# Optimization experiments

Measured on AMD Instinct MI355X. Metric: run time of the kernel, lower is better.

The kernel has to match this reference:

```python
import jax, jax.numpy as jnp
import numpy as np
jax.config.update("jax_enable_x64", True)  # faithful int64 spatial hashing as in torch

T = 524288            # hash table size per level
NL = jnp.asarray([16, 22, 30, 42, 58, 80, 110, 152, 209, 288, 397, 547, 754, 1039, 1432, 1974], dtype=jnp.float32)
L = 16
SCALE = 3.0
L_EMBED = 4
PI2 = 2654435761
PI3 = 805459861
NPTS = 524288

_k = np.arange(8)
# ceil/floor selector per original vertex enumeration, axis order (x, y, z)
CEIL_BITS = jnp.asarray(np.stack([
    [0, 1, 0, 0, 0, 1, 1, 1],   # x uses ceil
    [0, 0, 1, 0, 1, 0, 1, 1],   # y uses ceil
    [0, 0, 0, 1, 1, 1, 0, 1],   # z uses ceil
], axis=-1).astype(bool))        # [8,3]
# grid_sample places vertex k at grid (d,h,w)=(k//4,(k//2)%2,k%2); with align_corners=False
# on a 2x2x2 grid and grid coord frac-0.5, the weight for index 1 along W/H/D is frac_x/frac_y/frac_z.
# (This faithfully reproduces the original's vertex/weight mismatch.)
WEIGHT_BITS = jnp.asarray(np.stack([_k % 2, (_k // 2) % 2, _k // 4], axis=-1).astype(bool))  # [8,3]


def hash_features(xu, tables):
    # xu: [N,3] in ~[0,1]; tables: [L,T,2]
    def level(_, xs):
        n, table = xs
        p = xu * n
        pf = jnp.floor(p)
        pc = jnp.ceil(p)
        frac = p - pf                                                        # [N,3]
        verts = jnp.where(CEIL_BITS[None], pc[:, None, :], pf[:, None, :]).astype(jnp.int64)  # [N,8,3]
        h = ((verts[..., 0] * 1) ^ (verts[..., 1] * PI2) ^ (verts[..., 2] * PI3)) % T          # [N,8]
        w = jnp.prod(jnp.where(WEIGHT_BITS[None], frac[:, None, :], 1.0 - frac[:, None, :]), axis=-1)  # [N,8]
        feat = jnp.einsum('nk,nkf->nf', w.astype(table.dtype), table[h])    # [N,2]
        return None, feat
    _, feats = jax.lax.scan(level, None, (NL, tables))                       # [L,N,2]
    return jnp.transpose(feats, (1, 0, 2)).reshape(xu.shape[0], -1)          # [N,2L]


def posenc(d):
    outs = [d]
    for i in range(L_EMBED):
        s = (2.0 ** i) * d
        outs.append(jnp.sin(s))
        outs.append(jnp.cos(s))
    return jnp.concatenate(outs, -1)  # [N, 3+6*L_EMBED]


def setup_inputs() -> dict:
    key = jax.random.key(0)
    ks = jax.random.split(key, 16)
    f32 = jnp.float32
    s = 0.05
    return {
        "x": jax.random.normal(ks[0], (NPTS, 3), f32),
        "d": jax.random.normal(ks[1], (NPTS, 3), f32),
        "tables": (jax.random.uniform(ks[2], (L, T, 2), f32) * 2.0 - 1.0) * 1e-4,
        "w1a": jax.random.normal(ks[3], (2 * L, 64), f32) * s,
        "b1a": jnp.zeros((64,), f32),
        "w1b": jax.random.normal(ks[4], (64, 16), f32) * s,
        "b1b": jnp.zeros((16,), f32),
        "w2a": jax.random.normal(ks[5], (16 + 3 + 6 * L_EMBED, 64), f32) * s,
        "b2a": jnp.zeros((64,), f32),
        "w2b": jax.random.normal(ks[6], (64, 64), f32) * s,
        "b2b": jnp.zeros((64,), f32),
        "w2c": jax.random.normal(ks[7], (64, 3), f32) * s,
        "b2c": jnp.zeros((3,), f32),
    }


def reference(x, d, tables, w1a, b1a, w1b, b1b, w2a, b2a, w2b, b2b, w2c, b2c):
    xs = x / SCALE
    mask = (jnp.abs(xs[:, 0]) < 0.5) & (jnp.abs(xs[:, 1]) < 0.5) & (jnp.abs(xs[:, 2]) < 0.5)
    xu = xs + 0.5
    feats = hash_features(xu, tables)                     # [N, 32]
    h = jax.nn.relu(feats @ w1a + b1a) @ w1b + b1b        # [N, 16]
    log_sigma = jnp.where(mask, h[:, 0], -100000.0)
    z = jnp.concatenate([h, posenc(d)], -1)               # [N, 43]
    z = jax.nn.relu(z @ w2a + b2a)
    z = jax.nn.relu(z @ w2b + b2b)
    c = jax.nn.sigmoid(z @ w2c + b2c)
    color = jnp.where(mask[:, None], c, 0.0)
    return color, jnp.exp(log_sigma)
```

## Files before the change

kernel.cpp:

```cpp
#include <hip/hip_runtime.h>
#include <math.h>

#define NPTS 524288
#define HALF (NPTS / 2)
#define TSZ  524288
#define TMASK (TSZ - 1)
#define FP8SCALE 4096.0f
#define FP8INV   (1.0f / 4096.0f)

typedef __attribute__((ext_vector_type(8))) short v8s;
typedef __attribute__((ext_vector_type(4))) float v4f;
typedef __attribute__((ext_vector_type(2))) float v2f;

#define MFMA16(a, b, c) __builtin_amdgcn_mfma_f32_16x16x32_bf16(a, b, c, 0, 0, 0)

__device__ __constant__ float NLf[16] = {
    16.f, 22.f, 30.f, 42.f, 58.f, 80.f, 110.f, 152.f,
    209.f, 288.f, 397.f, 547.f, 754.f, 1039.f, 1432.f, 1974.f
};

#define CEILX 0xE2
#define CEILY 0xD4
#define CEILZ 0xB8

__device__ __forceinline__ short bf16r(float v) {
    unsigned b = __float_as_uint(v);
    b += 0x7FFFu + ((b >> 16) & 1u);
    return (short)(b >> 16);
}
__device__ __forceinline__ unsigned packbf(float a, float b) {
    return (unsigned)(unsigned short)bf16r(a) | ((unsigned)(unsigned short)bf16r(b) << 16);
}
__device__ __forceinline__ unsigned sel4(uint4 t, unsigned i) {
    const unsigned ab = (i & 1u) ? t.y : t.x;
    const unsigned cd = (i & 1u) ? t.w : t.z;
    return (i & 2u) ? cd : ab;
}
__device__ __forceinline__ unsigned sel8(uint4 t, unsigned i) {
    const unsigned w = sel4(t, i >> 1);
    return (i & 1u) ? (w >> 16) : (w & 0xFFFFu);
}

__global__ __launch_bounds__(256) void pack_tables(
    const float4* __restrict__ tbl, unsigned* __restrict__ out,
    unsigned* __restrict__ idxbuf, unsigned* __restrict__ cnt)
{
    const int idx = blockIdx.x * 256 + threadIdx.x;
    const float4 t = tbl[idx];
    const unsigned lo = (unsigned)__builtin_amdgcn_cvt_pk_fp8_f32(
                            t.x * FP8SCALE, t.y * FP8SCALE, 0, false) & 0xFFFFu;
    const unsigned hi = (unsigned)__builtin_amdgcn_cvt_pk_fp8_f32(
                            t.z * FP8SCALE, t.w * FP8SCALE, 0, false) & 0xFFFFu;
    out[idx] = lo | (hi << 16);
    if (idx < NPTS) idxbuf[idx] = 0xFFFFFFFFu;
    if (idx == 0) cnt[0] = 0u;
}

__global__ __launch_bounds__(1024) void ngp_compact2(
    const float* __restrict__ x, const float* __restrict__ d,
    unsigned* __restrict__ idxbuf, float* __restrict__ xc,
    float* __restrict__ dc, unsigned* __restrict__ cnt,
    float* __restrict__ out)
{
    __shared__ unsigned sWCnt[16];
    __shared__ unsigned sBase;

    const int tid  = threadIdx.x;
    const int wv   = tid >> 6, lane = tid & 63;
    const int i    = blockIdx.x * 1024 + tid;

    const float x0 = x[3*i+0], x1 = x[3*i+1], x2 = x[3*i+2];
    const float xs0 = x0 / 3.0f, xs1 = x1 / 3.0f, xs2 = x2 / 3.0f;
    const bool act = (fabsf(xs0) < 0.5f) && (fabsf(xs1) < 0.5f) && (fabsf(xs2) < 0.5f);
    if (!act) {
        out[3*i+0] = 0.f; out[3*i+1] = 0.f; out[3*i+2] = 0.f;
        out[3*NPTS + i] = 0.f;
    }
    const unsigned long long mb = __ballot(act);
    if (lane == 0) sWCnt[wv] = (unsigned)__popcll(mb);
    __syncthreads();
    if (tid == 0) {
        unsigned tot = 0;
        #pragma unroll
        for (int w = 0; w < 16; ++w) tot += sWCnt[w];
        sBase = atomicAdd(cnt, tot);
    }
    __syncthreads();
    if (act) {
        unsigned off = sBase;
        for (int w = 0; w < wv; ++w) off += sWCnt[w];
        off += (unsigned)__popcll(mb & ((1ull << lane) - 1ull));
        idxbuf[off] = (unsigned)i;
        xc[3*off+0] = x0; xc[3*off+1] = x1; xc[3*off+2] = x2;
        dc[3*off+0] = d[3*i+0]; dc[3*off+1] = d[3*i+1]; dc[3*off+2] = d[3*i+2];
    }
}

__global__ __launch_bounds__(256) void ngp_hash6(
    const float* __restrict__ xc, const unsigned short* __restrict__ tables_pk,
    const unsigned* __restrict__ cnt, unsigned* __restrict__ feats_pk)
{
    __shared__ float sX[768];
    const int NC = (int)cnt[0];
    if (blockIdx.x * 256 >= NC) return;

    const int tid = threadIdx.x;
    const int l = blockIdx.y;
    const float n = NLf[l];
    const unsigned short* tbl = tables_pk + (size_t)l * TSZ;

    for (int r = tid; r < 768; r += 256)
        sX[r] = xc[(size_t)blockIdx.x * 768 + r];
    __syncthreads();

    const int j = blockIdx.x * 256 + tid;
    const float xu0 = sX[tid * 3 + 0] / 3.0f + 0.5f;
    const float xu1 = sX[tid * 3 + 1] / 3.0f + 0.5f;
    const float xu2 = sX[tid * 3 + 2] / 3.0f + 0.5f;

    const float p0 = xu0 * n, p1 = xu1 * n, p2 = xu2 * n;
    const float f0 = floorf(p0), f1 = floorf(p1), f2 = floorf(p2);
    const float fr0 = p0 - f0, fr1 = p1 - f1, fr2 = p2 - f2;
    const float g0 = 1.f - fr0, g1 = 1.f - fr1, g2 = 1.f - fr2;
    const unsigned uvf0 = (unsigned)(int)f0;
    const unsigned uvc0 = (unsigned)(int)ceilf(p0);
    const unsigned syf = (unsigned)(int)f1 * 2654435761u;
    const unsigned syc = (unsigned)(int)ceilf(p1) * 2654435761u;
    const unsigned szf = (unsigned)(int)f2 * 805459861u;
    const unsigned szc = (unsigned)(int)ceilf(p2) * 805459861u;

    const float w0 = g0 * g1 * g2,  w1 = fr0 * g1 * g2;
    const float w2 = g0 * fr1 * g2, w6 = g0 * fr1 * fr2;
    const float w3 = fr0 * fr1 * g2, w5 = fr0 * g1 * fr2;
    const float w4 = g0 * g1 * fr2, w7 = fr0 * fr1 * fr2;

    const unsigned Ss[4] = { syf ^ szf, syc ^ szf, syf ^ szc, syc ^ szc };
    const float wf[4] = { w0, w2, w3, w4 };
    const float wc[4] = { w1, w6, w5, w7 };

    float a0 = 0.f, a1 = 0.f;
    #pragma unroll
    for (int pr = 0; pr < 4; ++pr) {
        const unsigned hf = (Ss[pr] ^ uvf0) & TMASK;
        const unsigned hc = (Ss[pr] ^ uvc0) & TMASK;
        const unsigned diff = hf ^ hc;
        const uint4 tv = *(const uint4*)(tbl + (hf & ~7u));
        const unsigned ef = sel8(tv, hf & 7u);
        unsigned ec;
        if (diff <= 7u) ec = sel8(tv, hc & 7u);
        else            ec = (unsigned)tbl[hc];
        const v2f ff = __builtin_amdgcn_cvt_pk_f32_fp8((int)ef, false);
        const v2f fc = __builtin_amdgcn_cvt_pk_f32_fp8((int)ec, false);
        a0 = fmaf(wf[pr], ff.x, a0);
        a1 = fmaf(wf[pr], ff.y, a1);
        a0 = fmaf(wc[pr], fc.x, a0);
        a1 = fmaf(wc[pr], fc.y, a1);
    }
    a0 *= FP8INV;
    a1 *= FP8INV;
    feats_pk[(size_t)l * NPTS + j] = packbf(a0, a1);
}

#define PZ 72
#define SWL(row) ((((row) >> 2) & 3) << 4)

__global__ __launch_bounds__(512) void ngp_mlp5(
    const float* __restrict__ dc,
    const unsigned* __restrict__ feats_pk, const unsigned* __restrict__ idxbuf,
    const unsigned* __restrict__ cnt,
    const float* __restrict__ w1a, const float* __restrict__ b1a,
    const float* __restrict__ w1b, const float* __restrict__ b1b,
    const float* __restrict__ w2a, const float* __restrict__ b2a,
    const float* __restrict__ w2b, const float* __restrict__ b2b,
    const float* __restrict__ w2c, const float* __restrict__ b2c,
    float* __restrict__ out)
{
    __shared__ short sW1a[64 * 40];
    __shared__ short sW1b[16 * 72];
    __shared__ short sW2a[64 * 72];
    __shared__ short sW2b[64 * 72];
    __shared__ short sW2c[16 * 72];
    __shared__ short sZ[8 * 16 * PZ];

    const int NC = (int)cnt[0];
    if (blockIdx.x * 128 >= NC) return;

    const int tid = threadIdx.x;

    for (int idx = tid; idx < 32 * 64; idx += 512) {
        const int k = idx >> 6, n2 = idx & 63;
        sW1a[n2 * 40 + k] = bf16r(w1a[k * 64 + n2]);
    }
    for (int idx = tid; idx < 64 * 16; idx += 512) {
        const int k = idx >> 4, n2 = idx & 15;
        sW1b[n2 * 72 + k] = bf16r(w1b[k * 16 + n2]);
    }
    for (int idx = tid; idx < 64 * 64; idx += 512) {
        const int k = idx >> 6, n2 = idx & 63;
        sW2a[n2 * 72 + k] = bf16r(k < 43 ? w2a[k * 64 + n2] : 0.f);
    }
    for (int idx = tid; idx < 64 * 64; idx += 512) {
        const int k = idx >> 6, n2 = idx & 63;
        sW2b[n2 * 72 + k] = bf16r(w2b[k * 64 + n2]);
    }
    for (int idx = tid; idx < 64 * 16; idx += 512) {
        const int k = idx >> 4, n2 = idx & 15;
        sW2c[n2 * 72 + k] = bf16r(n2 < 3 ? w2c[k * 3 + n2] : 0.f);
    }
    __syncthreads();

    const int wave = tid >> 6, lane = tid & 63;
    const int m = lane & 15, q = lane >> 4;
    short* zb = &sZ[wave * 16 * PZ];

    const int j0 = (blockIdx.x * 8 + wave) * 16;
    if (j0 >= NC) return;

    float bb1a[4], bb2a[4], bb2b[4];
    #pragma unroll
    for (int ct = 0; ct < 4; ++ct) {
        bb1a[ct] = b1a[ct * 16 + m];
        bb2a[ct] = b2a[ct * 16 + m];
        bb2b[ct] = b2b[ct * 16 + m];
    }
    const float bb1b = b1b[m];
    const float bb2c = (m < 3) ? b2c[m] : 0.f;

    #pragma unroll
    for (int it = 0; it < 4; ++it) {
        const int l = it * 4 + q;
        *(unsigned*)(zb + m * PZ + ((2 * l) ^ SWL(m))) =
            feats_pk[(size_t)l * NPTS + j0 + m];
    }

    {
        const v8s a0 = *(const v8s*)(zb + m * PZ + ((q * 8) ^ SWL(m)));
        #pragma unroll
        for (int ct = 0; ct < 4; ++ct) {
            const float bv = bb1a[ct];
            v4f acc = {bv, bv, bv, bv};
            acc = MFMA16(a0, *(const v8s*)(sW1a + (ct * 16 + m) * 40 + q * 8), acc);
            #pragma unroll
            for (int r = 0; r < 4; ++r)
                zb[(q * 4 + r) * PZ + ((ct * 16 + m) ^ (q << 4))] = bf16r(fmaxf(acc[r], 0.f));
        }
    }

    v4f hacc;
    {
        const v8s a10 = *(const v8s*)(zb + m * PZ + ((q * 8) ^ SWL(m)));
        const v8s a11 = *(const v8s*)(zb + m * PZ + ((32 + q * 8) ^ SWL(m)));
        v4f hv = {bb1b, bb1b, bb1b, bb1b};
        hv = MFMA16(a10, *(const v8s*)(sW1b + m * 72 + q * 8), hv);
        hv = MFMA16(a11, *(const v8s*)(sW1b + m * 72 + 32 + q * 8), hv);
        hacc = hv;
        #pragma unroll
        for (int r = 0; r < 4; ++r)
            zb[(q * 4 + r) * PZ + (m ^ (q << 4))] = bf16r(hv[r]);
    }

    {
        const float dd0 = dc[3*(j0+m)+0], dd1 = dc[3*(j0+m)+1], dd2 = dc[3*(j0+m)+2];
        v8s pk;
        #pragma unroll
        for (int jj = 0; jj < 8; ++jj) {
            const int k = 16 + q * 8 + jj;
            float v;
            if (k < 19) {
                v = (k == 16) ? dd0 : ((k == 17) ? dd1 : dd2);
            } else if (k < 43) {
                const int idx = k - 19;
                const int e = idx / 6, w = idx - 6 * e;
                const float base = (w == 0 || w == 3) ? dd0 : ((w == 1 || w == 4) ? dd1 : dd2);
                const float s = (float)(1 << e) * base;
                v = (w < 3) ? __sinf(s) : __cosf(s);
            } else {
                v = 0.f;
            }
            pk[jj] = bf16r(v);
        }
        *(v8s*)(zb + m * PZ + ((16 + q * 8) ^ SWL(m))) = pk;
        *(unsigned long long*)(zb + m * PZ + ((48 + q * 4) ^ SWL(m))) = 0ull;
    }

    {
        const v8s a20 = *(const v8s*)(zb + m * PZ + ((q * 8) ^ SWL(m)));
        const v8s a21 = *(const v8s*)(zb + m * PZ + ((32 + q * 8) ^ SWL(m)));
        #pragma unroll
        for (int ct = 0; ct < 4; ++ct) {
            const float bv = bb2a[ct];
            v4f acc = {bv, bv, bv, bv};
            acc = MFMA16(a20, *(const v8s*)(sW2a + (ct * 16 + m) * 72 + q * 8), acc);
            acc = MFMA16(a21, *(const v8s*)(sW2a + (ct * 16 + m) * 72 + 32 + q * 8), acc);
            #pragma unroll
            for (int r = 0; r < 4; ++r)
                zb[(q * 4 + r) * PZ + ((ct * 16 + m) ^ (q << 4))] = bf16r(fmaxf(acc[r], 0.f));
        }
    }

    {
        const v8s a20 = *(const v8s*)(zb + m * PZ + ((q * 8) ^ SWL(m)));
        const v8s a21 = *(const v8s*)(zb + m * PZ + ((32 + q * 8) ^ SWL(m)));
        #pragma unroll
        for (int ct = 0; ct < 4; ++ct) {
            const float bv = bb2b[ct];
            v4f acc = {bv, bv, bv, bv};
            acc = MFMA16(a20, *(const v8s*)(sW2b + (ct * 16 + m) * 72 + q * 8), acc);
            acc = MFMA16(a21, *(const v8s*)(sW2b + (ct * 16 + m) * 72 + 32 + q * 8), acc);
            #pragma unroll
            for (int r = 0; r < 4; ++r)
                zb[(q * 4 + r) * PZ + ((ct * 16 + m) ^ (q << 4))] = bf16r(fmaxf(acc[r], 0.f));
        }
    }

    {
        const v8s a30 = *(const v8s*)(zb + m * PZ + ((q * 8) ^ SWL(m)));
        const v8s a31 = *(const v8s*)(zb + m * PZ + ((32 + q * 8) ^ SWL(m)));
        v4f cacc = {bb2c, bb2c, bb2c, bb2c};
        cacc = MFMA16(a30, *(const v8s*)(sW2c + m * 72 + q * 8), cacc);
        cacc = MFMA16(a31, *(const v8s*)(sW2c + m * 72 + 32 + q * 8), cacc);

        if (m < 3) {
            #pragma unroll
            for (int r = 0; r < 4; ++r) {
                const unsigned pj = idxbuf[j0 + q * 4 + r];
                if (pj < (unsigned)NPTS) {
                    const float cv = 1.0f / (1.0f + __expf(-cacc[r]));
                    out[3 * pj + m] = cv;
                }
            }
        }
        if (m == 0) {
            #pragma unroll
            for (int r = 0; r < 4; ++r) {
                const unsigned pj = idxbuf[j0 + q * 4 + r];
                if (pj < (unsigned)NPTS)
                    out[3 * NPTS + pj] = __expf(hacc[r]);
            }
        }
    }
}

__global__ __launch_bounds__(256) void ngp_fused(
    const float* __restrict__ x, const float* __restrict__ d,
    const float* __restrict__ tables,
    const float* __restrict__ w1a, const float* __restrict__ b1a,
    const float* __restrict__ w1b, const float* __restrict__ b1b,
    const float* __restrict__ w2a, const float* __restrict__ b2a,
    const float* __restrict__ w2b, const float* __restrict__ b2b,
    const float* __restrict__ w2c, const float* __restrict__ b2c,
    float* __restrict__ out)
{
    const int i = blockIdx.x * 256 + threadIdx.x;
    if (i >= NPTS) return;
    const float xs0 = x[3*i+0] / 3.0f;
    const float xs1 = x[3*i+1] / 3.0f;
    const float xs2 = x[3*i+2] / 3.0f;
    const bool mask = (fabsf(xs0) < 0.5f) & (fabsf(xs1) < 0.5f) & (fabsf(xs2) < 0.5f);
    const float xu0 = xs0 + 0.5f, xu1 = xs1 + 0.5f, xu2 = xs2 + 0.5f;

    float feats[32];
    #pragma unroll
    for (int l = 0; l < 16; ++l) {
        const float n = NLf[l];
        const float p0 = xu0 * n, p1 = xu1 * n, p2 = xu2 * n;
        const float f0 = floorf(p0), f1 = floorf(p1), f2 = floorf(p2);
        const float fr0 = p0 - f0, fr1 = p1 - f1, fr2 = p2 - f2;
        const int vf0 = (int)f0, vf1 = (int)f1, vf2 = (int)f2;
        const int vc0 = (int)ceilf(p0), vc1 = (int)ceilf(p1), vc2 = (int)ceilf(p2);
        const float2* tbl = (const float2*)(tables + (size_t)l * (TSZ * 2));
        float a0 = 0.f, a1 = 0.f;
        #pragma unroll
        for (int k = 0; k < 8; ++k) {
            const unsigned vx = (unsigned)(((CEILX >> k) & 1) ? vc0 : vf0);
            const unsigned vy = (unsigned)(((CEILY >> k) & 1) ? vc1 : vf1);
            const unsigned vz = (unsigned)(((CEILZ >> k) & 1) ? vc2 : vf2);
            const unsigned h = (vx ^ (vy * 2654435761u) ^ (vz * 805459861u)) & TMASK;
            const float wx = (k & 1)        ? fr0 : 1.0f - fr0;
            const float wy = ((k >> 1) & 1) ? fr1 : 1.0f - fr1;
            const float wz = ((k >> 2) & 1) ? fr2 : 1.0f - fr2;
            const float wgt = wx * wy * wz;
            const float2 t = tbl[h];
            a0 = fmaf(wgt, t.x, a0);
            a1 = fmaf(wgt, t.y, a1);
        }
        feats[2*l] = a0; feats[2*l+1] = a1;
    }

    float h2v[16];
    #pragma unroll
    for (int j = 0; j < 16; ++j) h2v[j] = b1b[j];
    #pragma unroll
    for (int c = 0; c < 4; ++c) {
        float h1c[16];
        #pragma unroll
        for (int jj = 0; jj < 16; ++jj) h1c[jj] = b1a[16*c + jj];
        #pragma unroll
        for (int i2 = 0; i2 < 32; ++i2) {
            const float f = feats[i2];
            #pragma unroll
            for (int jj = 0; jj < 16; ++jj)
                h1c[jj] = fmaf(f, w1a[i2*64 + 16*c + jj], h1c[jj]);
        }
        #pragma unroll
        for (int jj = 0; jj < 16; ++jj) {
            const float f = fmaxf(h1c[jj], 0.f);
            #pragma unroll
            for (int t = 0; t < 16; ++t)
                h2v[t] = fmaf(f, w1b[(16*c + jj)*16 + t], h2v[t]);
        }
    }

    float z1[64];
    #pragma unroll
    for (int j = 0; j < 64; ++j) z1[j] = b2a[j];
    #pragma unroll
    for (int i2 = 0; i2 < 16; ++i2) {
        const float f = h2v[i2];
        #pragma unroll
        for (int j = 0; j < 64; ++j) z1[j] = fmaf(f, w2a[i2*64 + j], z1[j]);
    }
    const float d0 = d[3*i+0], d1 = d[3*i+1], d2 = d[3*i+2];
    {
        const float* r = w2a + 16*64;
        #pragma unroll
        for (int j = 0; j < 64; ++j) z1[j] = fmaf(d0, r[j], z1[j]);
        r = w2a + 17*64;
        #pragma unroll
        for (int j = 0; j < 64; ++j) z1[j] = fmaf(d1, r[j], z1[j]);
        r = w2a + 18*64;
        #pragma unroll
        for (int j = 0; j < 64; ++j) z1[j] = fmaf(d2, r[j], z1[j]);
    }
    #pragma unroll
    for (int e = 0; e < 4; ++e) {
        const float mm = (float)(1 << e);
        const float dv[3] = {d0, d1, d2};
        #pragma unroll
        for (int a = 0; a < 3; ++a) {
            const float sv = __sinf(mm * dv[a]);
            const float* rs = w2a + (19 + 6*e + a)*64;
            #pragma unroll
            for (int j = 0; j < 64; ++j) z1[j] = fmaf(sv, rs[j], z1[j]);
        }
        #pragma unroll
        for (int a = 0; a < 3; ++a) {
            const float cv = __cosf(mm * dv[a]);
            const float* rc = w2a + (19 + 6*e + 3 + a)*64;
            #pragma unroll
            for (int j = 0; j < 64; ++j) z1[j] = fmaf(cv, rc[j], z1[j]);
        }
    }
    #pragma unroll
    for (int j = 0; j < 64; ++j) z1[j] = fmaxf(z1[j], 0.f);

    float ca = b2c[0], cb = b2c[1], cc = b2c[2];
    #pragma unroll
    for (int jc = 0; jc < 64; jc += 16) {
        float acc[16];
        #pragma unroll
        for (int jj = 0; jj < 16; ++jj) acc[jj] = b2b[jc + jj];
        #pragma unroll
        for (int i2 = 0; i2 < 64; ++i2) {
            const float f = z1[i2];
            #pragma unroll
            for (int jj = 0; jj < 16; ++jj)
                acc[jj] = fmaf(f, w2b[i2*64 + jc + jj], acc[jj]);
        }
        #pragma unroll
        for (int jj = 0; jj < 16; ++jj) {
            const float v = fmaxf(acc[jj], 0.f);
            ca = fmaf(v, w2c[(jc + jj)*3 + 0], ca);
            cb = fmaf(v, w2c[(jc + jj)*3 + 1], cb);
            cc = fmaf(v, w2c[(jc + jj)*3 + 2], cc);
        }
    }

    float r = 1.0f / (1.0f + __expf(-ca));
    float g = 1.0f / (1.0f + __expf(-cb));
    float b = 1.0f / (1.0f + __expf(-cc));
    float sigma;
    if (mask) { sigma = __expf(h2v[0]); }
    else { r = 0.f; g = 0.f; b = 0.f; sigma = 0.f; }
    out[3*i + 0] = r;
    out[3*i + 1] = g;
    out[3*i + 2] = b;
    out[3*NPTS + i] = sigma;
}

extern "C" void kernel_launch(void* const* d_in, const int* in_sizes, int n_in,
                              void* d_out, int out_size, void* d_ws, size_t ws_size,
                              hipStream_t stream) {
    const float* x      = (const float*)d_in[0];
    const float* d      = (const float*)d_in[1];
    const float* tables = (const float*)d_in[2];
    const float* w1a    = (const float*)d_in[3];
    const float* b1a    = (const float*)d_in[4];
    const float* w1b    = (const float*)d_in[5];
    const float* b1b    = (const float*)d_in[6];
    const float* w2a    = (const float*)d_in[7];
    const float* b2a    = (const float*)d_in[8];
    const float* w2b    = (const float*)d_in[9];
    const float* b2b    = (const float*)d_in[10];
    const float* w2c    = (const float*)d_in[11];
    const float* b2c    = (const float*)d_in[12];
    float* out = (float*)d_out;

    const size_t need = (size_t)32 * NPTS * 4;
    if (ws_size >= need) {
        unsigned* base      = (unsigned*)d_ws;
        unsigned* feats_pk  = base;
        unsigned* tables_pk = base + (size_t)16 * NPTS;
        unsigned* idxbuf    = base + (size_t)24 * NPTS;
        unsigned* cnt       = base + (size_t)25 * NPTS;
        float*    xc        = (float*)(base + (size_t)26 * NPTS);
        float*    dc        = (float*)(base + (size_t)29 * NPTS);

        dim3 gp(16 * TSZ / (256 * 2)), bp(256);
        hipLaunchKernelGGL(pack_tables, gp, bp, 0, stream,
                           (const float4*)tables, tables_pk, idxbuf, cnt);

        dim3 gc(NPTS / 1024), bc(1024);
        hipLaunchKernelGGL(ngp_compact2, gc, bc, 0, stream,
                           x, d, idxbuf, xc, dc, cnt, out);

        dim3 gh(NPTS / 256, 16), bh(256);
        hipLaunchKernelGGL(ngp_hash6, gh, bh, 0, stream,
                           xc, (const unsigned short*)tables_pk, cnt, feats_pk);

        dim3 gm(NPTS / 128), bm(512);
        hipLaunchKernelGGL(ngp_mlp5, gm, bm, 0, stream,
                           dc, feats_pk, idxbuf, cnt, w1a, b1a, w1b, b1b,
                           w2a, b2a, w2b, b2b, w2c, b2c, out);
    } else {
        dim3 grid(NPTS / 256), block(256);
        hipLaunchKernelGGL(ngp_fused, grid, block, 0, stream,
                           x, d, tables, w1a, b1a, w1b, b1b,
                           w2a, b2a, w2b, b2b, w2c, b2c, out);
    }
}
```

Measured before the change: 268.7 us.

## Prepack MLP weights to bf16 once and loop multiple tiles per wave

Adds a small kernel that converts and transposes all MLP weights into a padded bf16 buffer, so each MLP block fills its shared memory with straight vector copies instead of strided float reads plus conversion. The MLP kernel now has each wave process four 16-point tiles in a loop, cutting the grid by four and spreading the weight-load cost over more points. This costs an extra kernel launch and fewer blocks, which may lower occupancy and latency hiding in the MLP stage.

```diff
diff --git a/kernel.cpp b/kernel.cpp
--- a/kernel.cpp
+++ b/kernel.cpp
@@ -54,6 +54,40 @@
     out[idx] = lo | (hi << 16);
     if (idx < NPTS) idxbuf[idx] = 0xFFFFFFFFu;
     if (idx == 0) cnt[0] = 0u;
+}
+
+#define W1A_OFF 0
+#define W1B_OFF 2560
+#define W2A_OFF 3712
+#define W2B_OFF 8320
+#define W2C_OFF 12928
+#define WPK_TOT 14080
+
+__global__ __launch_bounds__(1024) void ngp_packw(
+    const float* __restrict__ w1a, const float* __restrict__ w1b,
+    const float* __restrict__ w2a, const float* __restrict__ w2b,
+    const float* __restrict__ w2c, unsigned short* __restrict__ wpk)
+{
+    const int s = blockIdx.x * 1024 + threadIdx.x;
+    if (s >= WPK_TOT) return;
+    float v = 0.f;
+    if (s < W1B_OFF) {
+        const int r = s - W1A_OFF, n = r / 40, k = r % 40;
+        v = (k < 32) ? w1a[k * 64 + n] : 0.f;
+    } else if (s < W2A_OFF) {
+        const int r = s - W1B_OFF, n = r / 72, k = r % 72;
+        v = (k < 64) ? w1b[k * 16 + n] : 0.f;
+    } else if (s < W2B_OFF) {
+        const int r = s - W2A_OFF, n = r / 72, k = r % 72;
+        v = (k < 43) ? w2a[k * 64 + n] : 0.f;
+    } else if (s < W2C_OFF) {
+        const int r = s - W2B_OFF, n = r / 72, k = r % 72;
+        v = (k < 64) ? w2b[k * 64 + n] : 0.f;
+    } else {
+        const int r = s - W2C_OFF, n = r / 72, k = r % 72;
+        v = (k < 64 && n < 3) ? w2c[k * 3 + n] : 0.f;
+    }
+    wpk[s] = (unsigned short)bf16r(v);
 }
 
 __global__ __launch_bounds__(1024) void ngp_compact2(
@@ -164,57 +198,35 @@
 #define PZ 72
 #define SWL(row) ((((row) >> 2) & 3) << 4)
 
-__global__ __launch_bounds__(512) void ngp_mlp5(
+__global__ __launch_bounds__(512) void ngp_mlp6(
     const float* __restrict__ dc,
     const unsigned* __restrict__ feats_pk, const unsigned* __restrict__ idxbuf,
-    const unsigned* __restrict__ cnt,
-    const float* __restrict__ w1a, const float* __restrict__ b1a,
-    const float* __restrict__ w1b, const float* __restrict__ b1b,
-    const float* __restrict__ w2a, const float* __restrict__ b2a,
-    const float* __restrict__ w2b, const float* __restrict__ b2b,
-    const float* __restrict__ w2c, const float* __restrict__ b2c,
+    const unsigned* __restrict__ cnt, const unsigned short* __restrict__ wpk,
+    const float* __restrict__ b1a, const float* __restrict__ b1b,
+    const float* __restrict__ b2a, const float* __restrict__ b2b,
+    const float* __restrict__ b2c,
     float* __restrict__ out)
 {
-    __shared__ short sW1a[64 * 40];
-    __shared__ short sW1b[16 * 72];
-    __shared__ short sW2a[64 * 72];
-    __shared__ short sW2b[64 * 72];
-    __shared__ short sW2c[16 * 72];
+    __shared__ short sW[WPK_TOT];
     __shared__ short sZ[8 * 16 * PZ];
 
     const int NC = (int)cnt[0];
-    if (blockIdx.x * 128 >= NC) return;
+    if (blockIdx.x * 512 >= NC) return;
 
     const int tid = threadIdx.x;
-
-    for (int idx = tid; idx < 32 * 64; idx += 512) {
-        const int k = idx >> 6, n2 = idx & 63;
-        sW1a[n2 * 40 + k] = bf16r(w1a[k * 64 + n2]);
-    }
-    for (int idx = tid; idx < 64 * 16; idx += 512) {
-        const int k = idx >> 4, n2 = idx & 15;
-        sW1b[n2 * 72 + k] = bf16r(w1b[k * 16 + n2]);
-    }
-    for (int idx = tid; idx < 64 * 64; idx += 512) {
-        const int k = idx >> 6, n2 = idx & 63;
-        sW2a[n2 * 72 + k] = bf16r(k < 43 ? w2a[k * 64 + n2] : 0.f);
-    }
-    for (int idx = tid; idx < 64 * 64; idx += 512) {
-        const int k = idx >> 6, n2 = idx & 63;
-        sW2b[n2 * 72 + k] = bf16r(w2b[k * 64 + n2]);
-    }
-    for (int idx = tid; idx < 64 * 16; idx += 512) {
-        const int k = idx >> 4, n2 = idx & 15;
-        sW2c[n2 * 72 + k] = bf16r(n2 < 3 ? w2c[k * 3 + n2] : 0.f);
-    }
+    for (int i = tid; i < WPK_TOT / 8; i += 512)
+        ((uint4*)sW)[i] = ((const uint4*)wpk)[i];
     __syncthreads();
+
+    const short* sW1a = sW + W1A_OFF;
+    const short* sW1b = sW + W1B_OFF;
+    const short* sW2a = sW + W2A_OFF;
+    const short* sW2b = sW + W2B_OFF;
+    const short* sW2c = sW + W2C_OFF;
 
     const int wave = tid >> 6, lane = tid & 63;
     const int m = lane & 15, q = lane >> 4;
     short* zb = &sZ[wave * 16 * PZ];
-
-    const int j0 = (blockIdx.x * 8 + wave) * 16;
-    if (j0 >= NC) return;
 
     float bb1a[4], bb2a[4], bb2b[4];
     #pragma unroll
@@ -226,116 +238,123 @@
     const float bb1b = b1b[m];
     const float bb2c = (m < 3) ? b2c[m] : 0.f;
 
-    #pragma unroll
-    for (int it = 0; it < 4; ++it) {
-        const int l = it * 4 + q;
-        *(unsigned*)(zb + m * PZ + ((2 * l) ^ SWL(m))) =
-            feats_pk[(size_t)l * NPTS + j0 + m];
-    }
-
-    {
-        const v8s a0 = *(const v8s*)(zb + m * PZ + ((q * 8) ^ SWL(m)));
-        #pragma unroll
-        for (int ct = 0; ct < 4; ++ct) {
-            const float bv = bb1a[ct];
-            v4f acc = {bv, bv, bv, bv};
-            acc = MFMA16(a0, *(const v8s*)(sW1a + (ct * 16 + m) * 40 + q * 8), acc);
+    const int base = (blockIdx.x * 8 + wave) * 64;
+
+    for (int t = 0; t < 4; ++t) {
+        const int j0 = base + t * 16;
+        if (j0 >= NC) break;
+
+        #pragma unroll
+        for (int it = 0; it < 4; ++it) {
+            const int l = it * 4 + q;
+            *(unsigned*)(zb + m * PZ + ((2 * l) ^ SWL(m))) =
+                feats_pk[(size_t)l * NPTS + j0 + m];
+        }
+
+        {
+            const v8s a0 = *(const v8s*)(zb + m * PZ + ((q * 8) ^ SWL(m)));
+            #pragma unroll
+            for (int ct = 0; ct < 4; ++ct) {
+                const float bv = bb1a[ct];
+                v4f acc = {bv, bv, bv, bv};
+                acc = MFMA16(a0, *(const v8s*)(sW1a + (ct * 16 + m) * 40 + q * 8), acc);
+                #pragma unroll
+                for (int r = 0; r < 4; ++r)
+                    zb[(q * 4 + r) * PZ + ((ct * 16 + m) ^ (q << 4))] = bf16r(fmaxf(acc[r], 0.f));
+            }
+        }
+
+        v4f hacc;
+        {
+            const v8s a10 = *(const v8s*)(zb + m * PZ + ((q * 8) ^ SWL(m)));
+            const v8s a11 = *(const v8s*)(zb + m * PZ + ((32 + q * 8) ^ SWL(m)));
+            v4f hv = {bb1b, bb1b, bb1b, bb1b};
+            hv = MFMA16(a10, *(const v8s*)(sW1b + m * 72 + q * 8), hv);
+            hv = MFMA16(a11, *(const v8s*)(sW1b + m * 72 + 32 + q * 8), hv);
+            hacc = hv;
             #pragma unroll
             for (int r = 0; r < 4; ++r)
-                zb[(q * 4 + r) * PZ + ((ct * 16 + m) ^ (q << 4))] = bf16r(fmaxf(acc[r], 0.f));
-        }
-    }
-
-    v4f hacc;
-    {
-        const v8s a10 = *(const v8s*)(zb + m * PZ + ((q * 8) ^ SWL(m)));
-        const v8s a11 = *(const v8s*)(zb + m * PZ + ((32 + q * 8) ^ SWL(m)));
-        v4f hv = {bb1b, bb1b, bb1b, bb1b};
-        hv = MFMA16(a10, *(const v8s*)(sW1b + m * 72 + q * 8), hv);
-        hv = MFMA16(a11, *(const v8s*)(sW1b + m * 72 + 32 + q * 8), hv);
-        hacc = hv;
-        #pragma unroll
-        for (int r = 0; r < 4; ++r)
-            zb[(q * 4 + r) * PZ + (m ^ (q << 4))] = bf16r(hv[r]);
-    }
-
-    {
-        const float dd0 = dc[3*(j0+m)+0], dd1 = dc[3*(j0+m)+1], dd2 = dc[3*(j0+m)+2];
-        v8s pk;
-        #pragma unroll
-        for (int jj = 0; jj < 8; ++jj) {
-            const int k = 16 + q * 8 + jj;
-            float v;
-            if (k < 19) {
-                v = (k == 16) ? dd0 : ((k == 17) ? dd1 : dd2);
-            } else if (k < 43) {
-                const int idx = k - 19;
-                const int e = idx / 6, w = idx - 6 * e;
-                const float base = (w == 0 || w == 3) ? dd0 : ((w == 1 || w == 4) ? dd1 : dd2);
-                const float s = (float)(1 << e) * base;
-                v = (w < 3) ? __sinf(s) : __cosf(s);
-            } else {
-                v = 0.f;
+                zb[(q * 4 + r) * PZ + (m ^ (q << 4))] = bf16r(hv[r]);
+        }
+
+        {
+            const float dd0 = dc[3*(j0+m)+0], dd1 = dc[3*(j0+m)+1], dd2 = dc[3*(j0+m)+2];
+            v8s pk;
+            #pragma unroll
+            for (int jj = 0; jj < 8; ++jj) {
+                const int k = 16 + q * 8 + jj;
+                float v;
+                if (k < 19) {
+                    v = (k == 16) ? dd0 : ((k == 17) ? dd1 : dd2);
+                } else if (k < 43) {
+                    const int idx = k - 19;
+                    const int e = idx / 6, w = idx - 6 * e;
+                    const float base2 = (w == 0 || w == 3) ? dd0 : ((w == 1 || w == 4) ? dd1 : dd2);
+                    const float s = (float)(1 << e) * base2;
+                    v = (w < 3) ? __sinf(s) : __cosf(s);
+                } else {
+                    v = 0.f;
+                }
+                pk[jj] = bf16r(v);
             }
-            pk[jj] = bf16r(v);
-        }
-        *(v8s*)(zb + m * PZ + ((16 + q * 8) ^ SWL(m))) = pk;
-        *(unsigned long long*)(zb + m * PZ + ((48 + q * 4) ^ SWL(m))) = 0ull;
-    }
-
-    {
-        const v8s a20 = *(const v8s*)(zb + m * PZ + ((q * 8) ^ SWL(m)));
-        const v8s a21 = *(const v8s*)(zb + m * PZ + ((32 + q * 8) ^ SWL(m)));
-        #pragma unroll
-        for (int ct = 0; ct < 4; ++ct) {
-            const float bv = bb2a[ct];
-            v4f acc = {bv, bv, bv, bv};
-            acc = MFMA16(a20, *(const v8s*)(sW2a + (ct * 16 + m) * 72 + q * 8), acc);
-            acc = MFMA16(a21, *(const v8s*)(sW2a + (ct * 16 + m) * 72 + 32 + q * 8), acc);
-            #pragma unroll
-            for (int r = 0; r < 4; ++r)
-                zb[(q * 4 + r) * PZ + ((ct * 16 + m) ^ (q << 4))] = bf16r(fmaxf(acc[r], 0.f));
-        }
-    }
-
-    {
-        const v8s a20 = *(const v8s*)(zb + m * PZ + ((q * 8) ^ SWL(m)));
-        const v8s a21 = *(const v8s*)(zb + m * PZ + ((32 + q * 8) ^ SWL(m)));
-        #pragma unroll
-        for (int ct = 0; ct < 4; ++ct) {
-            const float bv = bb2b[ct];
-            v4f acc = {bv, bv, bv, bv};
-            acc = MFMA16(a20, *(const v8s*)(sW2b + (ct * 16 + m) * 72 + q * 8), acc);
-            acc = MFMA16(a21, *(const v8s*)(sW2b + (ct * 16 + m) * 72 + 32 + q * 8), acc);
-            #pragma unroll
-            for (int r = 0; r < 4; ++r)
-                zb[(q * 4 + r) * PZ + ((ct * 16 + m) ^ (q << 4))] = bf16r(fmaxf(acc[r], 0.f));
-        }
-    }
-
-    {
-        const v8s a30 = *(const v8s*)(zb + m * PZ + ((q * 8) ^ SWL(m)));
-        const v8s a31 = *(const v8s*)(zb + m * PZ + ((32 + q * 8) ^ SWL(m)));
-        v4f cacc = {bb2c, bb2c, bb2c, bb2c};
-        cacc = MFMA16(a30, *(const v8s*)(sW2c + m * 72 + q * 8), cacc);
-        cacc = MFMA16(a31, *(const v8s*)(sW2c + m * 72 + 32 + q * 8), cacc);
-
-        if (m < 3) {
-            #pragma unroll
-            for (int r = 0; r < 4; ++r) {
-                const unsigned pj = idxbuf[j0 + q * 4 + r];
-                if (pj < (unsigned)NPTS) {
-                    const float cv = 1.0f / (1.0f + __expf(-cacc[r]));
-                    out[3 * pj + m] = cv;
+            *(v8s*)(zb + m * PZ + ((16 + q * 8) ^ SWL(m))) = pk;
+            *(unsigned long long*)(zb + m * PZ + ((48 + q * 4) ^ SWL(m))) = 0ull;
+        }
+
+        {
+            const v8s a20 = *(const v8s*)(zb + m * PZ + ((q * 8) ^ SWL(m)));
+            const v8s a21 = *(const v8s*)(zb + m * PZ + ((32 + q * 8) ^ SWL(m)));
+            #pragma unroll
+            for (int ct = 0; ct < 4; ++ct) {
+                const float bv = bb2a[ct];
+                v4f acc = {bv, bv, bv, bv};
+                acc = MFMA16(a20, *(const v8s*)(sW2a + (ct * 16 + m) * 72 + q * 8), acc);
+                acc = MFMA16(a21, *(const v8s*)(sW2a + (ct * 16 + m) * 72 + 32 + q * 8), acc);
+                #pragma unroll
+                for (int r = 0; r < 4; ++r)
+                    zb[(q * 4 + r) * PZ + ((ct * 16 + m) ^ (q << 4))] = bf16r(fmaxf(acc[r], 0.f));
+            }
+        }
+
+        {
+            const v8s a20 = *(const v8s*)(zb + m * PZ + ((q * 8) ^ SWL(m)));
+            const v8s a21 = *(const v8s*)(zb + m * PZ + ((32 + q * 8) ^ SWL(m)));
+            #pragma unroll
+            for (int ct = 0; ct < 4; ++ct) {
+                const float bv = bb2b[ct];
+                v4f acc = {bv, bv, bv, bv};
+                acc = MFMA16(a20, *(const v8s*)(sW2b + (ct * 16 + m) * 72 + q * 8), acc);
+                acc = MFMA16(a21, *(const v8s*)(sW2b + (ct * 16 + m) * 72 + 32 + q * 8), acc);
+                #pragma unroll
+                for (int r = 0; r < 4; ++r)
+                    zb[(q * 4 + r) * PZ + ((ct * 16 + m) ^ (q << 4))] = bf16r(fmaxf(acc[r], 0.f));
+            }
+        }
+
+        {
+            const v8s a30 = *(const v8s*)(zb + m * PZ + ((q * 8) ^ SWL(m)));
+            const v8s a31 = *(const v8s*)(zb + m * PZ + ((32 + q * 8) ^ SWL(m)));
+            v4f cacc = {bb2c, bb2c, bb2c, bb2c};
+            cacc = MFMA16(a30, *(const v8s*)(sW2c + m * 72 + q * 8), cacc);
+            cacc = MFMA16(a31, *(const v8s*)(sW2c + m * 72 + 32 + q * 8), cacc);
+
+            if (m < 3) {
+                #pragma unroll
+                for (int r = 0; r < 4; ++r) {
+                    const unsigned pj = idxbuf[j0 + q * 4 + r];
+                    if (pj < (unsigned)NPTS) {
+                        const float cv = 1.0f / (1.0f + __expf(-cacc[r]));
+                        out[3 * pj + m] = cv;
+                    }
                 }
             }
-        }
-        if (m == 0) {
-            #pragma unroll
-            for (int r = 0; r < 4; ++r) {
-                const unsigned pj = idxbuf[j0 + q * 4 + r];
-                if (pj < (unsigned)NPTS)
-                    out[3 * NPTS + pj] = __expf(hacc[r]);
+            if (m == 0) {
+                #pragma unroll
+                for (int r = 0; r < 4; ++r) {
+                    const unsigned pj = idxbuf[j0 + q * 4 + r];
+                    if (pj < (unsigned)NPTS)
+                        out[3 * NPTS + pj] = __expf(hacc[r]);
+                }
             }
         }
     }
@@ -506,7 +525,7 @@
     const float* b2c    = (const float*)d_in[12];
     float* out = (float*)d_out;
 
-    const size_t need = (size_t)32 * NPTS * 4;
+    const size_t need = (size_t)33 * NPTS * 4;
     if (ws_size >= need) {
         unsigned* base      = (unsigned*)d_ws;
         unsigned* feats_pk  = base;
@@ -515,11 +534,16 @@
         unsigned* cnt       = base + (size_t)25 * NPTS;
         float*    xc        = (float*)(base + (size_t)26 * NPTS);
         float*    dc        = (float*)(base + (size_t)29 * NPTS);
+        unsigned short* wpk = (unsigned short*)(base + (size_t)32 * NPTS);
 
         dim3 gp(16 * TSZ / (256 * 2)), bp(256);
         hipLaunchKernelGGL(pack_tables, gp, bp, 0, stream,
                            (const float4*)tables, tables_pk, idxbuf, cnt);
 
+        dim3 gw((WPK_TOT + 1023) / 1024), bw(1024);
+        hipLaunchKernelGGL(ngp_packw, gw, bw, 0, stream,
+                           w1a, w1b, w2a, w2b, w2c, wpk);
+
         dim3 gc(NPTS / 1024), bc(1024);
         hipLaunchKernelGGL(ngp_compact2, gc, bc, 0, stream,
                            x, d, idxbuf, xc, dc, cnt, out);
@@ -528,10 +552,10 @@
         hipLaunchKernelGGL(ngp_hash6, gh, bh, 0, stream,
                            xc, (const unsigned short*)tables_pk, cnt, feats_pk);
 
-        dim3 gm(NPTS / 128), bm(512);
-        hipLaunchKernelGGL(ngp_mlp5, gm, bm, 0, stream,
-                           dc, feats_pk, idxbuf, cnt, w1a, b1a, w1b, b1b,
-                           w2a, b2a, w2b, b2b, w2c, b2c, out);
+        dim3 gm(NPTS / 512), bm(512);
+        hipLaunchKernelGGL(ngp_mlp6, gm, bm, 0, stream,
+                           dc, feats_pk, idxbuf, cnt, wpk,
+                           b1a, b1b, b2a, b2b, b2c, out);
     } else {
         dim3 grid(NPTS / 256), block(256);
         hipLaunchKernelGGL(ngp_fused, grid, block, 0, stream,
```

Result: no change. 265.1 us (-1.4%).
